# Optimization experiments

Hardware: AMD Instinct MI355X
Metric: run time of the kernel (lower is better)

Reference implementation:

```python
import jax, jax.numpy as jnp
import numpy as np

NUM_HEADS = 4
EPS = 1e-5


def conv1(W, b, z):
    # Conv1d with kernel_size=1 == channel-wise linear: (B, Cin, L) -> (B, Cout, L)
    return jnp.einsum('oi,bil->bol', W, z) + b[None, :, None]


def setup_inputs() -> dict:
    key = jax.random.key(0)
    ks = jax.random.split(key, 16)
    B, D, N = 2, 256, 4096
    s = 0.05
    return {
        'x': jax.random.normal(ks[0], (B, D, N), jnp.float32),
        'source': jax.random.normal(ks[1], (B, D, N), jnp.float32),
        'Wq': jax.random.normal(ks[2], (D, D), jnp.float32) * s,
        'bq': jax.random.normal(ks[3], (D,), jnp.float32) * s,
        'Wk': jax.random.normal(ks[4], (D, D), jnp.float32) * s,
        'bk': jax.random.normal(ks[5], (D,), jnp.float32) * s,
        'Wv': jax.random.normal(ks[6], (D, D), jnp.float32) * s,
        'bv': jax.random.normal(ks[7], (D,), jnp.float32) * s,
        'Wm': jax.random.normal(ks[8], (D, D), jnp.float32) * s,
        'bm': jax.random.normal(ks[9], (D,), jnp.float32) * s,
        'W1': jax.random.normal(ks[10], (2 * D, 2 * D), jnp.float32) * s,
        'b1': jax.random.normal(ks[11], (2 * D,), jnp.float32) * s,
        'W2': jax.random.normal(ks[12], (D, 2 * D), jnp.float32) * s,
        'b2': jax.random.normal(ks[13], (D,), jnp.float32) * s,
    }


def reference(x, source, Wq, bq, Wk, bk, Wv, bv, Wm, bm, W1, b1, W2, b2):
    B, D, N = x.shape
    M = source.shape[2]
    H = NUM_HEADS
    dim = D // H  # per-head dim; torch reshape splits channels as (dim, heads)

    q = conv1(Wq, bq, x).reshape(B, dim, H, N)
    k = conv1(Wk, bk, source).reshape(B, dim, H, M)
    v = conv1(Wv, bv, source).reshape(B, dim, H, M)

    scores = jnp.einsum('bdhn,bdhm->bhnm', q, k) / (dim ** 0.5)
    prob = jax.nn.softmax(scores, axis=-1)
    attn = jnp.einsum('bhnm,bdhm->bdhn', prob, v).reshape(B, D, N)

    message = conv1(Wm, bm, attn)

    h = conv1(W1, b1, jnp.concatenate([x, message], axis=1))
    # InstanceNorm1d (affine=False, biased var over L)
    mu = jnp.mean(h, axis=2, keepdims=True)
    var = jnp.mean((h - mu) ** 2, axis=2, keepdims=True)
    h = jax.nn.relu((h - mu) / jnp.sqrt(var + EPS))
    return conv1(W2, b2, h)
```

## Files before the change

kernel.cpp:

```cpp
#include <hip/hip_runtime.h>
#include <cstdint>
#include <cstddef>


typedef __attribute__((ext_vector_type(8))) short short8;
typedef __attribute__((ext_vector_type(4))) float floatx4;

__device__ __forceinline__ unsigned short f2bf(float x) {
  union { float f; unsigned int u; } c; c.f = x;
  unsigned int r = c.u + 0x7FFFu + ((c.u >> 16) & 1u);
  return (unsigned short)(r >> 16);
}
__device__ __forceinline__ float bf2f(unsigned short u) {
  union { unsigned int i; float f; } c; c.i = ((unsigned int)u) << 16; return c.f;
}
__device__ __forceinline__ void gload16(const void* g, void* l) {
  __builtin_amdgcn_global_load_lds(
      (const __attribute__((address_space(1))) unsigned int*)g,
      (__attribute__((address_space(3))) unsigned int*)l, 16, 0, 0);
}

#define LOG2E_8 0.18033688011112042f

__global__ __launch_bounds__(256) void tx_all(
    const float* __restrict__ x, const float* __restrict__ src,
    unsigned short* __restrict__ xb, unsigned short* __restrict__ sb,
    int C, int N)
{
  __shared__ float tile[32][33];
  const int which = blockIdx.z >> 1, b = blockIdx.z & 1;
  const float* X = which ? src : x;
  unsigned short* Y = which ? sb : xb;
  const int n0 = blockIdx.x * 32, c0 = blockIdx.y * 32;
  const int tc = threadIdx.x & 31, tr = threadIdx.x >> 5;
  #pragma unroll
  for (int i = 0; i < 4; ++i)
    tile[tr + i * 8][tc] = X[((size_t)b * C + c0 + tr + i * 8) * N + n0 + tc];
  __syncthreads();
  #pragma unroll
  for (int i = 0; i < 4; ++i)
    Y[((size_t)b * N + n0 + tr + i * 8) * C + c0 + tc] = f2bf(tile[tc][tr + i * 8]);
}

__global__ __launch_bounds__(256) void wprep(
    const float* __restrict__ Wq, const float* __restrict__ Wk,
    const float* __restrict__ Wv, const float* __restrict__ Wm,
    const float* __restrict__ W1, const float* __restrict__ W2,
    const float* __restrict__ bq, const float* __restrict__ bk,
    const float* __restrict__ bv, const float* __restrict__ bm,
    const float* __restrict__ b1, const float* __restrict__ b2,
    unsigned short* __restrict__ wqkv, unsigned short* __restrict__ wm_,
    unsigned short* __restrict__ w1_, unsigned short* __restrict__ w2_,
    float* __restrict__ biasb)
{
  const int bid = blockIdx.x, t = threadIdx.x;
  if (bid < 768) {
    const int idx = bid * 256 + t;
    const int op = idx >> 8, ip = idx & 255;
    const int grp = op >> 8, oo = op & 255;
    const int o = 4 * (oo & 63) + (oo >> 6);
    const float* W = grp == 0 ? Wq : grp == 1 ? Wk : Wv;
    const float sc = grp == 0 ? LOG2E_8 : 1.f;
    wqkv[idx] = f2bf(W[(size_t)o * 256 + ip] * sc);
  } else if (bid < 1024) {
    const int idx = (bid - 768) * 256 + t;
    const int op = idx >> 8, ip = idx & 255;
    const int i2 = 4 * (ip & 63) + (ip >> 6);
    wm_[idx] = f2bf(Wm[(size_t)op * 256 + i2]);
  } else if (bid < 2048) {
    const int idx = (bid - 1024) * 256 + t;
    w1_[idx] = f2bf(W1[idx]);
  } else if (bid < 2560) {
    const int idx = (bid - 2048) * 256 + t;
    w2_[idx] = f2bf(W2[idx]);
  } else {
    const int z = (bid - 2560) * 256 + t;
    if (z < 256)       biasb[z] = bq[4 * (z & 63) + (z >> 6)] * LOG2E_8;
    else if (z < 512)  { const int y = z - 256; biasb[z] = bk[4 * (y & 63) + (y >> 6)]; }
    else if (z < 768)  { const int y = z - 512; biasb[z] = bv[4 * (y & 63) + (y >> 6)]; }
    else if (z < 1024) biasb[z] = bm[z - 768];
    else if (z < 1536) biasb[z] = b1[z - 1024];
    else if (z < 1792) biasb[z] = b2[z - 1536];
  }
}

__global__ __launch_bounds__(256) void gemm128(
    const unsigned short* __restrict__ Wb, const float* __restrict__ bias,
    const unsigned short* __restrict__ X0, const unsigned short* __restrict__ X1,
    void* __restrict__ O0, void* __restrict__ O1, void* __restrict__ O2,
    int Co, int Ci, int Ci0, int N, int variant)
{
  const int n0 = blockIdx.x * 128;
  const int o0 = blockIdx.y * 128;
  const int b  = blockIdx.z;
  const int t  = threadIdx.x;
  const int w = t >> 6, lane = t & 63, qd = lane >> 4, l = lane & 15;
  const int oh = (w >> 1) * 64, nh = (w & 1) * 64;

  __shared__ unsigned short Wl[128 * 64];
  __shared__ unsigned short Xl[128 * 64];

  floatx4 acc[4][4];
  #pragma unroll
  for (int i = 0; i < 4; ++i)
    #pragma unroll
    for (int j = 0; j < 4; ++j) acc[i][j] = (floatx4){0.f, 0.f, 0.f, 0.f};

  for (int k0 = 0; k0 < Ci; k0 += 64) {
    const unsigned short* Xs; int cb, rl;
    if (variant == 1) { Xs = (o0 < 256) ? X0 : X1; cb = k0; rl = Ci; }
    else if (k0 < Ci0) { Xs = X0; cb = k0; rl = Ci0; }
    else               { Xs = X1; cb = k0 - Ci0; rl = Ci - Ci0; }
    __syncthreads();
    #pragma unroll
    for (int i = 0; i < 4; ++i) {
      const int idx = i * 256 + t;
      const int row = idx >> 3, pg = idx & 7, sg = pg ^ (row & 7);
      gload16(&Wb[(size_t)(o0 + row) * Ci + k0 + sg * 8], &Wl[row * 64 + pg * 8]);
      gload16(&Xs[((size_t)b * N + n0 + row) * rl + cb + sg * 8], &Xl[row * 64 + pg * 8]);
    }
    __syncthreads();

    short8 af[4][2], bf[4][2];
    #pragma unroll
    for (int i = 0; i < 4; ++i) {
      const int ar = oh + 16 * i + l;
      af[i][0] = *(const short8*)&Wl[ar * 64 + ((qd ^ (ar & 7))) * 8];
      af[i][1] = *(const short8*)&Wl[ar * 64 + (((4 + qd) ^ (ar & 7))) * 8];
    }
    #pragma unroll
    for (int j = 0; j < 4; ++j) {
      const int br = nh + 16 * j + l;
      bf[j][0] = *(const short8*)&Xl[br * 64 + ((qd ^ (br & 7))) * 8];
      bf[j][1] = *(const short8*)&Xl[br * 64 + (((4 + qd) ^ (br & 7))) * 8];
    }
    #pragma unroll
    for (int i = 0; i < 4; ++i)
      #pragma unroll
      for (int j = 0; j < 4; ++j) {
        acc[i][j] = __builtin_amdgcn_mfma_f32_16x16x32_bf16(af[i][0], bf[j][0], acc[i][j], 0, 0, 0);
        acc[i][j] = __builtin_amdgcn_mfma_f32_16x16x32_bf16(af[i][1], bf[j][1], acc[i][j], 0, 0, 0);
      }
  }

  const int osec = o0 + oh;
  #pragma unroll
  for (int i = 0; i < 4; ++i) {
    const int o4 = o0 + oh + 16 * i + qd * 4;
    const float4 bi = *(const float4*)&bias[o4];
    #pragma unroll
    for (int j = 0; j < 4; ++j) {
      const int n = n0 + nh + 16 * j + l;
      if (variant == 0) {
        unsigned short* C = (unsigned short*)O0;
        ushort4 pk;
        pk.x = f2bf(acc[i][j][0] + bi.x); pk.y = f2bf(acc[i][j][1] + bi.y);
        pk.z = f2bf(acc[i][j][2] + bi.z); pk.w = f2bf(acc[i][j][3] + bi.w);
        *(ushort4*)&C[((size_t)b * N + n) * Co + o4] = pk;
      } else if (variant == 1) {
        if (osec < 256) {
          unsigned short* C = (unsigned short*)O0;
          ushort4 pk;
          pk.x = f2bf(acc[i][j][0] + bi.x); pk.y = f2bf(acc[i][j][1] + bi.y);
          pk.z = f2bf(acc[i][j][2] + bi.z); pk.w = f2bf(acc[i][j][3] + bi.w);
          *(ushort4*)&C[((size_t)b * N + n) * 256 + o4] = pk;
        } else if (osec < 512) {
          unsigned short* C = (unsigned short*)O1;
          ushort4 pk;
          pk.x = f2bf(acc[i][j][0] + bi.x); pk.y = f2bf(acc[i][j][1] + bi.y);
          pk.z = f2bf(acc[i][j][2] + bi.z); pk.w = f2bf(acc[i][j][3] + bi.w);
          *(ushort4*)&C[((size_t)b * N + n) * 256 + (o4 - 256)] = pk;
        } else {
          unsigned short* C = (unsigned short*)O2;
          #pragma unroll
          for (int rg = 0; rg < 4; ++rg) {
            const int op = o4 - 512 + rg, h = op >> 6, d = op & 63;
            C[(((size_t)b * 4 + h) * 64 + d) * N + n] =
                f2bf(acc[i][j][rg] + ((const float*)&bi)[rg]);
          }
        }
      } else {
        float* C = (float*)O0;
        #pragma unroll
        for (int rg = 0; rg < 4; ++rg)
          C[((size_t)b * Co + o4 + rg) * N + n] = acc[i][j][rg] + ((const float*)&bi)[rg];
      }
    }
  }
}

__global__ __launch_bounds__(256) void attn_mfma(
    const unsigned short* __restrict__ qb, const unsigned short* __restrict__ kb,
    const unsigned short* __restrict__ vh, unsigned short* __restrict__ Opart,
    float* __restrict__ liPart, int N)
{
  const int qt = blockIdx.x;
  const int h  = blockIdx.y;
  const int b  = blockIdx.z >> 2, s = blockIdx.z & 3;
  const int n0 = qt * 128;
  const int t  = threadIdx.x;
  const int w = t >> 6, lane = t & 63, qd = lane >> 4, l = lane & 15;

  __shared__ unsigned short Kl[64 * 64];
  __shared__ unsigned short Vl[64 * 64];
  __shared__ unsigned short Pl[4][16 * 64];

  const unsigned short* qp0 = &qb[((size_t)b * N + n0 + 16 * w + l) * 256 + h * 64];
  const unsigned short* qp1 = qp0 + (size_t)64 * 256;
  short8 aQ[2][2];
  aQ[0][0] = *(const short8*)&qp0[qd * 8];
  aQ[0][1] = *(const short8*)&qp0[32 + qd * 8];
  aQ[1][0] = *(const short8*)&qp1[qd * 8];
  aQ[1][1] = *(const short8*)&qp1[32 + qd * 8];

  floatx4 accO[2][4];
  #pragma unroll
  for (int qs = 0; qs < 2; ++qs)
    #pragma unroll
    for (int ds = 0; ds < 4; ++ds) accO[qs][ds] = (floatx4){0.f, 0.f, 0.f, 0.f};
  float li[2][4] = {};

  const int j0base = s * 1024;
  for (int jt = 0; jt < 16; ++jt) {
    const int j0 = j0base + jt * 64;
    __syncthreads();
    #pragma unroll
    for (int i = 0; i < 2; ++i) {
      const int idx = i * 256 + t;
      const int row = idx >> 3, pg = idx & 7, sg = pg ^ (row & 7);
      gload16(&kb[((size_t)b * N + j0 + row) * 256 + h * 64 + sg * 8],
              &Kl[row * 64 + pg * 8]);
      gload16(&vh[(((size_t)b * 4 + h) * 64 + row) * N + j0 + sg * 8],
              &Vl[row * 64 + pg * 8]);
    }
    __syncthreads();

    short8 kf[4][2], vf[4][2];
    #pragma unroll
    for (int js = 0; js < 4; ++js) {
      const int br = 16 * js + l;
      kf[js][0] = *(const short8*)&Kl[br * 64 + ((qd ^ (br & 7))) * 8];
      kf[js][1] = *(const short8*)&Kl[br * 64 + (((4 + qd) ^ (br & 7))) * 8];
      vf[js][0] = *(const short8*)&Vl[br * 64 + ((qd ^ (br & 7))) * 8];
      vf[js][1] = *(const short8*)&Vl[br * 64 + (((4 + qd) ^ (br & 7))) * 8];
    }

    #pragma unroll
    for (int qs = 0; qs < 2; ++qs) {
      floatx4 S[4];
      #pragma unroll
      for (int js = 0; js < 4; ++js) {
        floatx4 a = (floatx4){0.f, 0.f, 0.f, 0.f};
        a = __builtin_amdgcn_mfma_f32_16x16x32_bf16(aQ[qs][0], kf[js][0], a, 0, 0, 0);
        a = __builtin_amdgcn_mfma_f32_16x16x32_bf16(aQ[qs][1], kf[js][1], a, 0, 0, 0);
        S[js] = a;
      }
      #pragma unroll
      for (int js = 0; js < 4; ++js) {
        const int kg = 2 * js + (l >> 3);
        #pragma unroll
        for (int rg = 0; rg < 4; ++rg) {
          const float p = __builtin_exp2f(S[js][rg]);
          li[qs][rg] += p;
          union { float f; unsigned int u; } cv; cv.f = p;
          const int qr = qd * 4 + rg;
          Pl[w][qr * 64 + ((kg ^ (qr & 7))) * 8 + (l & 7)] =
              (unsigned short)((cv.u + 0x8000u) >> 16);
        }
      }
      const short8 aP0 = *(const short8*)&Pl[w][l * 64 + ((qd ^ (l & 7))) * 8];
      const short8 aP1 = *(const short8*)&Pl[w][l * 64 + (((4 + qd) ^ (l & 7))) * 8];
      #pragma unroll
      for (int ds = 0; ds < 4; ++ds) {
        accO[qs][ds] = __builtin_amdgcn_mfma_f32_16x16x32_bf16(aP0, vf[ds][0], accO[qs][ds], 0, 0, 0);
        accO[qs][ds] = __builtin_amdgcn_mfma_f32_16x16x32_bf16(aP1, vf[ds][1], accO[qs][ds], 0, 0, 0);
      }
    }
  }

  const size_t obase = ((((size_t)b * 4 + h) * 4 + s) * 32 + qt) * 128;
  #pragma unroll
  for (int qs = 0; qs < 2; ++qs)
    #pragma unroll
    for (int rg = 0; rg < 4; ++rg) {
      float sum = li[qs][rg];
      sum += __shfl_xor(sum, 1);
      sum += __shfl_xor(sum, 2);
      sum += __shfl_xor(sum, 4);
      sum += __shfl_xor(sum, 8);
      const int q = qs * 64 + 16 * w + qd * 4 + rg;
      #pragma unroll
      for (int ds = 0; ds < 4; ++ds)
        Opart[(obase + q) * 64 + 16 * ds + l] = f2bf(accO[qs][ds][rg]);
      if (l == 0) liPart[obase + q] = sum;
    }
}

__global__ __launch_bounds__(256) void attn_combine(
    const unsigned short* __restrict__ Opart, const float* __restrict__ liPart,
    unsigned short* __restrict__ atb, int N)
{
  const int qt = blockIdx.x, h = blockIdx.y, b = blockIdx.z;
  const int t = threadIdx.x;
  const int q = t >> 1, d0 = (t & 1) * 32;

  float li = 0.f;
  size_t idx[4];
  #pragma unroll
  for (int s = 0; s < 4; ++s) {
    idx[s] = ((((size_t)b * 4 + h) * 4 + s) * 32 + qt) * 128 + q;
    li += liPart[idx[s]];
  }
  const float inv = 1.f / li;

  float o[32];
  #pragma unroll
  for (int c = 0; c < 32; ++c) o[c] = 0.f;
  #pragma unroll
  for (int s = 0; s < 4; ++s) {
    #pragma unroll
    for (int c4 = 0; c4 < 4; ++c4) {
      const short8 v = *(const short8*)&Opart[idx[s] * 64 + d0 + c4 * 8];
      #pragma unroll
      for (int j = 0; j < 8; ++j) o[c4 * 8 + j] += bf2f((unsigned short)v[j]);
    }
  }
  unsigned short* dst = &atb[((size_t)b * N + qt * 128 + q) * 256 + h * 64 + d0];
  #pragma unroll
  for (int c4 = 0; c4 < 4; ++c4) {
    ushort4 pk;
    pk.x = f2bf(o[c4 * 8 + 0] * inv); pk.y = f2bf(o[c4 * 8 + 1] * inv);
    pk.z = f2bf(o[c4 * 8 + 2] * inv); pk.w = f2bf(o[c4 * 8 + 3] * inv);
    *(ushort4*)&dst[c4 * 8] = pk;
    pk.x = f2bf(o[c4 * 8 + 4] * inv); pk.y = f2bf(o[c4 * 8 + 5] * inv);
    pk.z = f2bf(o[c4 * 8 + 6] * inv); pk.w = f2bf(o[c4 * 8 + 7] * inv);
    *(ushort4*)&dst[c4 * 8 + 4] = pk;
  }
}

__global__ __launch_bounds__(256) void in_stats(
    const unsigned short* __restrict__ H, float* __restrict__ Ps,
    float* __restrict__ Ps2, int N)
{
  const int cg = blockIdx.x, ns = blockIdx.y, b = blockIdx.z, t = threadIdx.x;
  const int c0 = cg * 64 + (t & 7) * 8;
  float s[8] = {}, s2[8] = {};
  #pragma unroll
  for (int i = 0; i < 8; ++i) {
    const int n = ns * 256 + (t >> 3) + i * 32;
    const short8 hv = *(const short8*)&H[((size_t)b * N + n) * 512 + c0];
    #pragma unroll
    for (int j = 0; j < 8; ++j) {
      const float f = bf2f((unsigned short)hv[j]);
      s[j] += f; s2[j] += f * f;
    }
  }
  __shared__ float rs[32][64], rs2[32][64];
  #pragma unroll
  for (int j = 0; j < 8; ++j) {
    rs[t >> 3][(t & 7) * 8 + j] = s[j];
    rs2[t >> 3][(t & 7) * 8 + j] = s2[j];
  }
  __syncthreads();
  if (t < 64) {
    float a = 0.f, a2 = 0.f;
    #pragma unroll
    for (int r = 0; r < 32; ++r) { a += rs[r][t]; a2 += rs2[r][t]; }
    const size_t o = ((size_t)ns * 2 + b) * 512 + cg * 64 + t;
    Ps[o] = a; Ps2[o] = a2;
  }
}

__global__ __launch_bounds__(256) void in_norm(
    unsigned short* __restrict__ H, const float* __restrict__ Ps,
    const float* __restrict__ Ps2, int N)
{
  const int cg = blockIdx.x, ns = blockIdx.y, b = blockIdx.z, t = threadIdx.x;
  __shared__ float muS[64], ivS[64];
  if (t < 64) {
    const int c = cg * 64 + t;
    float s = 0.f, s2 = 0.f;
    for (int k = 0; k < 16; ++k) {
      s  += Ps [((size_t)k * 2 + b) * 512 + c];
      s2 += Ps2[((size_t)k * 2 + b) * 512 + c];
    }
    const float mu = s / (float)N;
    const float var = fmaxf(s2 / (float)N - mu * mu, 0.f);
    muS[t] = mu;
    ivS[t] = rsqrtf(var + 1e-5f);
  }
  __syncthreads();
  const int c0 = cg * 64 + (t & 7) * 8;
  float mu[8], iv[8];
  #pragma unroll
  for (int j = 0; j < 8; ++j) {
    mu[j] = muS[(t & 7) * 8 + j];
    iv[j] = ivS[(t & 7) * 8 + j];
  }
  #pragma unroll
  for (int i = 0; i < 8; ++i) {
    const int n = ns * 256 + (t >> 3) + i * 32;
    unsigned short* p = &H[((size_t)b * N + n) * 512 + c0];
    short8 hv = *(const short8*)p;
    #pragma unroll
    for (int j = 0; j < 8; ++j) {
      const float f = fmaxf((bf2f((unsigned short)hv[j]) - mu[j]) * iv[j], 0.f);
      hv[j] = (short)f2bf(f);
    }
    *(short8*)p = hv;
  }
}

extern "C" void kernel_launch(void* const* d_in, const int* in_sizes, int n_in,
                              void* d_out, int out_size, void* d_ws, size_t ws_size,
                              hipStream_t stream)
{
  const int B = 2, D = 256, N = 4096;

  const float* x   = (const float*)d_in[0];
  const float* src = (const float*)d_in[1];
  const float* Wq  = (const float*)d_in[2];  const float* bq = (const float*)d_in[3];
  const float* Wk  = (const float*)d_in[4];  const float* bk = (const float*)d_in[5];
  const float* Wv  = (const float*)d_in[6];  const float* bv = (const float*)d_in[7];
  const float* Wm  = (const float*)d_in[8];  const float* bm = (const float*)d_in[9];
  const float* W1  = (const float*)d_in[10]; const float* b1 = (const float*)d_in[11];
  const float* W2  = (const float*)d_in[12]; const float* b2 = (const float*)d_in[13];
  float* out = (float*)d_out;

  char* ws = (char*)d_ws;
  const size_t MB = 1u << 20;
  unsigned short* xb  = (unsigned short*)(ws + 0 * MB);
  unsigned short* sb  = (unsigned short*)(ws + 4 * MB);
  unsigned short* qbf = (unsigned short*)(ws + 8 * MB);
  unsigned short* kbf = (unsigned short*)(ws + 12 * MB);
  unsigned short* vhb = (unsigned short*)(ws + 16 * MB);
  unsigned short* atb = (unsigned short*)(ws + 20 * MB);
  unsigned short* Opart = (unsigned short*)(ws + 24 * MB);
  unsigned short* msb = (unsigned short*)(ws + 24 * MB);
  unsigned short* hb  = (unsigned short*)(ws + 28 * MB);
  float* liPart = (float*)(ws + 41 * MB);
  unsigned short* wqkvb = (unsigned short*)(ws + 42 * MB);
  unsigned short* wmb = wqkvb + 768 * 256;
  unsigned short* w1b = wmb + 256 * 256;
  unsigned short* w2b = w1b + 512 * 512;
  float* biasb = (float*)(ws + 44 * MB);
  float* Ps    = biasb + 2048;
  float* Ps2   = Ps + 16 * 2 * 512;

  const dim3 blk(256);

  tx_all<<<dim3(N / 32, D / 32, 2 * B), blk, 0, stream>>>(x, src, xb, sb, D, N);
  wprep<<<dim3(2567), blk, 0, stream>>>(Wq, Wk, Wv, Wm, W1, W2,
                                        bq, bk, bv, bm, b1, b2,
                                        wqkvb, wmb, w1b, w2b, biasb);

  gemm128<<<dim3(N / 128, 6, B), blk, 0, stream>>>(
      wqkvb, biasb, xb, sb, qbf, kbf, vhb, 768, 256, 256, N, 1);

  attn_mfma<<<dim3(N / 128, 4, B * 4), blk, 0, stream>>>(
      qbf, kbf, vhb, Opart, liPart, N);
  attn_combine<<<dim3(N / 128, 4, B), blk, 0, stream>>>(Opart, liPart, atb, N);

  gemm128<<<dim3(N / 128, 2, B), blk, 0, stream>>>(
      wmb, biasb + 768, atb, atb, msb, nullptr, nullptr, 256, 256, 256, N, 0);

  gemm128<<<dim3(N / 128, 4, B), blk, 0, stream>>>(
      w1b, biasb + 1024, xb, msb, hb, nullptr, nullptr, 512, 512, 256, N, 0);

  in_stats<<<dim3(8, 16, B), blk, 0, stream>>>(hb, Ps, Ps2, N);
  in_norm<<<dim3(8, 16, B), blk, 0, stream>>>(hb, Ps, Ps2, N);

  gemm128<<<dim3(N / 128, 2, B), blk, 0, stream>>>(
      w2b, biasb + 1536, hb, hb, out, nullptr, nullptr, 256, 512, 512, N, 2);
}
```

Baseline: 236.5 us.

## Double-buffer K/V tiles and keep softmax probabilities in registers for PV MFMA

The attention kernel now double-buffers the K and V LDS tiles, so the next tile's global-to-LDS load is issued while the current tile is being computed, and only one barrier is needed per iteration. The QK^T product is computed transposed (K as the A operand), so each lane holds four consecutive keys for one query. Those probabilities are packed to bf16 with v_cvt_pk_bf16_f32 and fed directly to 16x16x16 MFMAs, which removes the per-wave P scratch round-trip through LDS and the per-row shuffle reduction. s_setprio hints are added around the MFMA blocks. In exchange, LDS use for K/V doubles and the P·V step issues more, smaller MFMA instructions.

```diff
diff --git a/kernel.cpp b/kernel.cpp
--- a/kernel.cpp
+++ b/kernel.cpp
@@ -4,7 +4,10 @@
 
 
 typedef __attribute__((ext_vector_type(8))) short short8;
+typedef __attribute__((ext_vector_type(4))) short bf16x4;
 typedef __attribute__((ext_vector_type(4))) float floatx4;
+
+union U2 { unsigned int u[2]; bf16x4 s; };
 
 __device__ __forceinline__ unsigned short f2bf(float x) {
   union { float f; unsigned int u; } c; c.f = x;
@@ -18,6 +21,19 @@
   __builtin_amdgcn_global_load_lds(
       (const __attribute__((address_space(1))) unsigned int*)g,
       (__attribute__((address_space(3))) unsigned int*)l, 16, 0, 0);
+}
+__device__ __forceinline__ unsigned int cvtpk(float lo, float hi) {
+  unsigned int r;
+  asm("v_cvt_pk_bf16_f32 %0, %1, %2" : "=v"(r) : "v"(lo), "v"(hi));
+  return r;
+}
+__device__ __forceinline__ floatx4 mfma16(bf16x4 a, bf16x4 b, floatx4 c) {
+#if __has_builtin(__builtin_amdgcn_mfma_f32_16x16x16bf16_1k)
+  return __builtin_amdgcn_mfma_f32_16x16x16bf16_1k(a, b, c, 0, 0, 0);
+#else
+  asm("v_mfma_f32_16x16x16_bf16 %0, %1, %2, %0" : "+v"(c) : "v"(a), "v"(b));
+  return c;
+#endif
 }
 
 #define LOG2E_8 0.18033688011112042f
@@ -201,99 +217,114 @@
   const int t  = threadIdx.x;
   const int w = t >> 6, lane = t & 63, qd = lane >> 4, l = lane & 15;
 
-  __shared__ unsigned short Kl[64 * 64];
-  __shared__ unsigned short Vl[64 * 64];
-  __shared__ unsigned short Pl[4][16 * 64];
+  __shared__ unsigned short Kl[2][64 * 64];
+  __shared__ unsigned short Vl[2][64 * 64];
 
   const unsigned short* qp0 = &qb[((size_t)b * N + n0 + 16 * w + l) * 256 + h * 64];
   const unsigned short* qp1 = qp0 + (size_t)64 * 256;
-  short8 aQ[2][2];
-  aQ[0][0] = *(const short8*)&qp0[qd * 8];
-  aQ[0][1] = *(const short8*)&qp0[32 + qd * 8];
-  aQ[1][0] = *(const short8*)&qp1[qd * 8];
-  aQ[1][1] = *(const short8*)&qp1[32 + qd * 8];
+  short8 bQ[2][2];
+  bQ[0][0] = *(const short8*)&qp0[qd * 8];
+  bQ[0][1] = *(const short8*)&qp0[32 + qd * 8];
+  bQ[1][0] = *(const short8*)&qp1[qd * 8];
+  bQ[1][1] = *(const short8*)&qp1[32 + qd * 8];
 
   floatx4 accO[2][4];
   #pragma unroll
   for (int qs = 0; qs < 2; ++qs)
     #pragma unroll
     for (int ds = 0; ds < 4; ++ds) accO[qs][ds] = (floatx4){0.f, 0.f, 0.f, 0.f};
-  float li[2][4] = {};
+  float li[2] = {0.f, 0.f};
 
   const int j0base = s * 1024;
-  for (int jt = 0; jt < 16; ++jt) {
-    const int j0 = j0base + jt * 64;
-    __syncthreads();
+
+  auto STAGE = [&](int buf, int j0) {
     #pragma unroll
     for (int i = 0; i < 2; ++i) {
       const int idx = i * 256 + t;
       const int row = idx >> 3, pg = idx & 7, sg = pg ^ (row & 7);
       gload16(&kb[((size_t)b * N + j0 + row) * 256 + h * 64 + sg * 8],
-              &Kl[row * 64 + pg * 8]);
+              &Kl[buf][row * 64 + pg * 8]);
       gload16(&vh[(((size_t)b * 4 + h) * 64 + row) * N + j0 + sg * 8],
-              &Vl[row * 64 + pg * 8]);
-    }
+              &Vl[buf][row * 64 + pg * 8]);
+    }
+  };
+
+  STAGE(0, j0base);
+
+  #pragma unroll 2
+  for (int jt = 0; jt < 16; ++jt) {
+    const int cur = jt & 1;
     __syncthreads();
-
-    short8 kf[4][2], vf[4][2];
+    if (jt < 15) STAGE(cur ^ 1, j0base + (jt + 1) * 64);
+
+    short8 kf[4][2];
     #pragma unroll
     for (int js = 0; js < 4; ++js) {
       const int br = 16 * js + l;
-      kf[js][0] = *(const short8*)&Kl[br * 64 + ((qd ^ (br & 7))) * 8];
-      kf[js][1] = *(const short8*)&Kl[br * 64 + (((4 + qd) ^ (br & 7))) * 8];
-      vf[js][0] = *(const short8*)&Vl[br * 64 + ((qd ^ (br & 7))) * 8];
-      vf[js][1] = *(const short8*)&Vl[br * 64 + (((4 + qd) ^ (br & 7))) * 8];
+      kf[js][0] = *(const short8*)&Kl[cur][br * 64 + ((qd ^ (br & 7))) * 8];
+      kf[js][1] = *(const short8*)&Kl[cur][br * 64 + (((4 + qd) ^ (br & 7))) * 8];
+    }
+    bf16x4 vf[4][4];
+    #pragma unroll
+    for (int ds = 0; ds < 4; ++ds) {
+      const int vr = 16 * ds + l;
+      #pragma unroll
+      for (int js = 0; js < 4; ++js) {
+        const int pg = js * 2 + (qd >> 1);
+        vf[ds][js] = *(const bf16x4*)&Vl[cur][vr * 64 + ((pg ^ (vr & 7))) * 8 + (qd & 1) * 4];
+      }
     }
 
     #pragma unroll
     for (int qs = 0; qs < 2; ++qs) {
       floatx4 S[4];
+      __builtin_amdgcn_s_setprio(1);
       #pragma unroll
       for (int js = 0; js < 4; ++js) {
         floatx4 a = (floatx4){0.f, 0.f, 0.f, 0.f};
-        a = __builtin_amdgcn_mfma_f32_16x16x32_bf16(aQ[qs][0], kf[js][0], a, 0, 0, 0);
-        a = __builtin_amdgcn_mfma_f32_16x16x32_bf16(aQ[qs][1], kf[js][1], a, 0, 0, 0);
+        a = __builtin_amdgcn_mfma_f32_16x16x32_bf16(kf[js][0], bQ[qs][0], a, 0, 0, 0);
+        a = __builtin_amdgcn_mfma_f32_16x16x32_bf16(kf[js][1], bQ[qs][1], a, 0, 0, 0);
         S[js] = a;
       }
+      __builtin_amdgcn_s_setprio(0);
+
+      bf16x4 pa[4];
       #pragma unroll
       for (int js = 0; js < 4; ++js) {
-        const int kg = 2 * js + (l >> 3);
+        const float p0 = __builtin_exp2f(S[js][0]);
+        const float p1 = __builtin_exp2f(S[js][1]);
+        const float p2 = __builtin_exp2f(S[js][2]);
+        const float p3 = __builtin_exp2f(S[js][3]);
+        li[qs] += (p0 + p1) + (p2 + p3);
+        U2 pu; pu.u[0] = cvtpk(p0, p1); pu.u[1] = cvtpk(p2, p3);
+        pa[js] = pu.s;
+      }
+
+      __builtin_amdgcn_s_setprio(1);
+      #pragma unroll
+      for (int ds = 0; ds < 4; ++ds)
         #pragma unroll
-        for (int rg = 0; rg < 4; ++rg) {
-          const float p = __builtin_exp2f(S[js][rg]);
-          li[qs][rg] += p;
-          union { float f; unsigned int u; } cv; cv.f = p;
-          const int qr = qd * 4 + rg;
-          Pl[w][qr * 64 + ((kg ^ (qr & 7))) * 8 + (l & 7)] =
-              (unsigned short)((cv.u + 0x8000u) >> 16);
-        }
-      }
-      const short8 aP0 = *(const short8*)&Pl[w][l * 64 + ((qd ^ (l & 7))) * 8];
-      const short8 aP1 = *(const short8*)&Pl[w][l * 64 + (((4 + qd) ^ (l & 7))) * 8];
-      #pragma unroll
-      for (int ds = 0; ds < 4; ++ds) {
-        accO[qs][ds] = __builtin_amdgcn_mfma_f32_16x16x32_bf16(aP0, vf[ds][0], accO[qs][ds], 0, 0, 0);
-        accO[qs][ds] = __builtin_amdgcn_mfma_f32_16x16x32_bf16(aP1, vf[ds][1], accO[qs][ds], 0, 0, 0);
-      }
+        for (int js = 0; js < 4; ++js)
+          accO[qs][ds] = mfma16(pa[js], vf[ds][js], accO[qs][ds]);
+      __builtin_amdgcn_s_setprio(0);
     }
   }
 
   const size_t obase = ((((size_t)b * 4 + h) * 4 + s) * 32 + qt) * 128;
   #pragma unroll
-  for (int qs = 0; qs < 2; ++qs)
+  for (int qs = 0; qs < 2; ++qs) {
+    float sum = li[qs];
+    sum += __shfl_xor(sum, 16);
+    sum += __shfl_xor(sum, 32);
+    if (qd == 0) liPart[obase + qs * 64 + 16 * w + l] = sum;
     #pragma unroll
     for (int rg = 0; rg < 4; ++rg) {
-      float sum = li[qs][rg];
-      sum += __shfl_xor(sum, 1);
-      sum += __shfl_xor(sum, 2);
-      sum += __shfl_xor(sum, 4);
-      sum += __shfl_xor(sum, 8);
       const int q = qs * 64 + 16 * w + qd * 4 + rg;
       #pragma unroll
       for (int ds = 0; ds < 4; ++ds)
         Opart[(obase + q) * 64 + 16 * ds + l] = f2bf(accO[qs][ds][rg]);
-      if (l == 0) liPart[obase + q] = sum;
-    }
+    }
+  }
 }
 
 __global__ __launch_bounds__(256) void attn_combine(
```

Result: faster. 231.4 us (-2.1%).
